# Kernel tuning notes

Hardware: AMD Instinct MI355X
Metric: run time of the kernel (lower is better)

## Reference

```python
import jax, jax.numpy as jnp
import numpy as np

N_SITE, D, PHYS, W = 40, 128, 2, 8  # sites, MPS bond dim, physical dim, MPO bond dim


def setup_inputs() -> dict:
    key = jax.random.key(0)
    k1, k2 = jax.random.split(key)
    # scale so 40-step transfer-matrix products stay O(1) in float32
    M = jax.random.normal(k1, (N_SITE, D, PHYS, D), jnp.float32) * (D * PHYS) ** -0.5
    H = jax.random.normal(k2, (N_SITE, W, W, PHYS, PHYS), jnp.float32) * (W * PHYS * PHYS) ** -0.5
    return {"M": M, "H": H}


def _energy(M, H):
    # <M|H|M> via left-to-right environment sweep. L has shape (D_bra, w, D_ket).
    L0 = jnp.zeros((D, W, D), M.dtype).at[0, 0, 0].set(1.0)  # open left boundary

    def step(L, mh):
        m, h = mh  # m: (a,i,p) bond,phys,bond ; h: (w,x,i,j) mpo-bond,mpo-bond,phys-out,phys-in
        T = jnp.einsum('awb,aip->wbip', L, m)      # absorb bra tensor (real, so no conj)
        T = jnp.einsum('wbip,wxij->bpxj', T, h)    # absorb MPO tensor
        L = jnp.einsum('bpxj,bjq->pxq', T, m)      # absorb ket tensor
        return L, None

    L, _ = jax.lax.scan(step, L0, (M, H))
    return L[0, W - 1, 0]  # open right boundary (MPO right boundary = last index)


def _norm(M):
    # <M|M> via transfer-matrix sweep. N has shape (D_bra, D_ket); stays PSD.
    N0 = jnp.zeros((D, D), M.dtype).at[0, 0].set(1.0)

    def step(N, m):
        T = jnp.einsum('ab,aip->bip', N, m)
        N = jnp.einsum('bip,biq->pq', T, m)
        return N, None

    N, _ = jax.lax.scan(step, N0, M)
    return N[0, 0]


def reference(M, H):
    EPS = 0.0
    NORM_LIM = 10000.0
    energy = _energy(M, H)
    norm = _norm(M)
    loss = energy / (norm + EPS)  # torch.real is identity for real dtype
    reg = jax.nn.relu(norm - NORM_LIM)
    return (energy, norm, loss, reg)
```

## Files before the change

### kernel.cpp

```cpp
#include <hip/hip_runtime.h>


#define D 128
#define W 8
#define NS 40
#define NPAIR 20
#define HALF2 10
#define MSZ (D * 2 * D)
#define HSZ (W * W * 2 * 2)
#define M2SZ (D * 4 * D)
#define H2SZ (W * W * 4 * 4)
#define LSZ (D * W * D)
#define NSZ (D * D)
#define T2SZ (D * W * D * 4)
#define TNSZ (4 * D * D)

#define OFF_M2 0
#define OFF_MR2 (OFF_M2 + NPAIR * M2SZ)
#define OFF_H2 (OFF_MR2 + HALF2 * M2SZ)
#define OFF_HR2 (OFF_H2 + NPAIR * H2SZ)
#define OFF_LL (OFF_HR2 + HALF2 * H2SZ)
#define OFF_LR (OFF_LL + LSZ)
#define OFF_NL (OFF_LR + LSZ)
#define OFF_NR (OFF_NL + NSZ)
#define OFF_T2L (OFF_NR + NSZ)
#define OFF_T2R (OFF_T2L + T2SZ)
#define OFF_TNL (OFF_T2R + T2SZ)
#define OFF_TNR (OFF_TNL + TNSZ)
#define OFF_PART (OFF_TNR + TNSZ)
#define OFF_PARTN (OFF_PART + 128)

__global__ __launch_bounds__(256) void k_prep1(const float* __restrict__ Min,
                                               const float* __restrict__ Hin,
                                               float* __restrict__ ws) {
    __shared__ float As[32 * 34];
    __shared__ float Bs[32 * 68];
    int bid = blockIdx.x, t = threadIdx.x;
    if (bid < 640) {
        int m = bid >> 5, tile = bid & 31;
        int r0 = (tile & 7) * 32, c0 = (tile >> 3) * 64;
        const float* A = Min + (2 * m) * MSZ;
        const float* B = Min + (2 * m + 1) * MSZ;
        float* C = ws + OFF_M2 + m * M2SZ;
        int ty = t >> 4, tx = t & 15;
        float a00 = 0, a01 = 0, a02 = 0, a03 = 0;
        float a10 = 0, a11 = 0, a12 = 0, a13 = 0;
        for (int c = 0; c < 4; ++c) {
            int k0 = c * 32;
            __syncthreads();
            {
                int rr = t >> 3, kq = t & 7;
                int row = r0 + rr;
                const float4 v = *(const float4*)&A[(row >> 1) * 256 + (row & 1) * 128 + k0 + kq * 4];
                float* dst = &As[kq * 136 + rr];
                dst[0] = v.x; dst[34] = v.y; dst[68] = v.z; dst[102] = v.w;
            }
#pragma unroll
            for (int u = 0; u < 2; ++u) {
                int e = u * 256 + t;
                int kk = e >> 4, cq = e & 15;
                const float4 v = *(const float4*)&B[(k0 + kk) * 256 + c0 + cq * 4];
                *(float4*)&Bs[kk * 68 + cq * 4] = v;
            }
            __syncthreads();
#pragma unroll 8
            for (int kk = 0; kk < 32; ++kk) {
                float2 av = *(float2*)&As[kk * 34 + 2 * ty];
                float4 bv = *(float4*)&Bs[kk * 68 + 4 * tx];
                a00 += av.x * bv.x; a01 += av.x * bv.y; a02 += av.x * bv.z; a03 += av.x * bv.w;
                a10 += av.y * bv.x; a11 += av.y * bv.y; a12 += av.y * bv.z; a13 += av.y * bv.w;
            }
        }
        int r = r0 + 2 * ty, cc = c0 + 4 * tx;
        int a = r >> 1, i2 = cc >> 7, cd = cc & 127;
        float4 v0; v0.x = a00; v0.y = a01; v0.z = a02; v0.w = a03;
        float4 v1; v1.x = a10; v1.y = a11; v1.z = a12; v1.w = a13;
        *(float4*)&C[a * 512 + (0 * 2 + i2) * 128 + cd] = v0;
        *(float4*)&C[a * 512 + (1 * 2 + i2) * 128 + cd] = v1;
    } else {
        for (int idx = t; idx < NPAIR * H2SZ; idx += 256) {
            int m = idx >> 10, r = idx & 1023;
            int w = r >> 7, x = (r >> 4) & 7, I = (r >> 2) & 3, J = r & 3;
            int i1 = I >> 1, i2 = I & 1, j1 = J >> 1, j2 = J & 1;
            const float* Ha = Hin + (2 * m) * HSZ;
            const float* Hb = Hin + (2 * m + 1) * HSZ;
            float s = 0.f;
#pragma unroll
            for (int v = 0; v < 8; ++v)
                s += Ha[w * 32 + v * 4 + i1 * 2 + j1] * Hb[v * 32 + x * 4 + i2 * 2 + j2];
            ws[OFF_H2 + idx] = s;
        }
    }
}

#define PR_MR (HALF2 * M2SZ)
#define PR_HR (PR_MR + HALF2 * H2SZ)
#define PR_TOT (PR_HR + 2 * LSZ + 2 * NSZ)
__global__ __launch_bounds__(256) void k_prep2(float* __restrict__ ws) {
    for (int idx = blockIdx.x * 256 + threadIdx.x; idx < PR_TOT; idx += gridDim.x * 256) {
        if (idx < PR_MR) {
            int kr = idx >> 16, r = idx & 65535;
            int a = r >> 9, I = (r >> 7) & 3, p = r & 127;
            ws[OFF_MR2 + idx] = ws[OFF_M2 + (19 - kr) * M2SZ + p * 512 + I * 128 + a];
        } else if (idx < PR_HR) {
            int e = idx - PR_MR;
            int kr = e >> 10, r = e & 1023;
            int w = r >> 7, x = (r >> 4) & 7, lo = r & 15;
            ws[OFF_HR2 + e] = ws[OFF_H2 + (19 - kr) * H2SZ + x * 128 + w * 16 + lo];
        } else {
            int e = idx - PR_HR;
            int off; float v = 0.f;
            if (e < LSZ)            { off = OFF_LL + e; if (e == 0) v = 1.f; }
            else if (e < 2 * LSZ)   { int r = e - LSZ; off = OFF_LR + r; if (r == (W - 1) * D) v = 1.f; }
            else if (e < 2 * LSZ + NSZ) { int r = e - 2 * LSZ; off = OFF_NL + r; if (r == 0) v = 1.f; }
            else                    { int r = e - 2 * LSZ - NSZ; off = OFF_NR + r; if (r == 0) v = 1.f; }
            ws[off] = v;
        }
    }
}

__global__ __launch_bounds__(512) void k_A2(float* __restrict__ ws, int k) {
    __shared__ __align__(16) float sm[9472];
    int bid = blockIdx.x, t = threadIdx.x;
    int z = t >> 8, tl = t & 255;
    if (bid < 128) {
        int side = bid >> 6;
        int eb = bid & 63;
        int b0 = (eb & 7) * 16;
        int p0 = (eb >> 3) * 16;
        const float* Lsrc = ws + (side ? OFF_LR : OFF_LL);
        const float* m2 = ws + (side ? OFF_MR2 : OFF_M2) + k * M2SZ;
        const float* h2 = ws + (side ? OFF_HR2 : OFF_H2) + k * H2SZ;
        float* T2 = ws + (side ? OFF_T2R : OFF_T2L);
        float* Ls = sm;
        float* ms = sm + 6400;
        float* hs = sm + 8448;
#pragma unroll
        for (int u = 0; u < 2; ++u) {
            int e = u * 512 + t;
            int w = e >> 7, I = (e >> 5) & 3, x = (e >> 2) & 7, J = e & 3;
            hs[e] = h2[w * 128 + x * 16 + I * 4 + J];
        }
        int b_l = tl & 15, p_l = tl >> 4;
        float acc[8][2];
#pragma unroll
        for (int w = 0; w < 8; ++w) { acc[w][0] = 0.f; acc[w][1] = 0.f; }
        int e0 = t, e1 = 512 + t;
        int la0 = e0 >> 5, lw0 = (e0 >> 2) & 7, lb0 = e0 & 3;
        int la1 = e1 >> 5, lw1 = (e1 >> 2) & 7, lb1 = e1 & 3;
        int maa = t >> 4, mI = (t >> 2) & 3, mpq = t & 3;
        float4 pl0 = *(const float4*)&Lsrc[la0 * 1024 + lw0 * 128 + b0 + lb0 * 4];
        float4 pl1 = *(const float4*)&Lsrc[la1 * 1024 + lw1 * 128 + b0 + lb1 * 4];
        float4 pm = *(const float4*)&m2[maa * 512 + mI * 128 + p0 + mpq * 4];
        for (int c = 0; c < 4; ++c) {
            __syncthreads();
            {
                float* d0 = &Ls[la0 * 200 + lb0 * 48 + lw0];
                d0[0] = pl0.x; d0[12] = pl0.y; d0[24] = pl0.z; d0[36] = pl0.w;
                float* d1 = &Ls[la1 * 200 + lb1 * 48 + lw1];
                d1[0] = pl1.x; d1[12] = pl1.y; d1[24] = pl1.z; d1[36] = pl1.w;
                *(float4*)&ms[maa * 64 + mI * 16 + mpq * 4] = pm;
            }
            if (c < 3) {
                int a0 = (c + 1) * 32;
                pl0 = *(const float4*)&Lsrc[(a0 + la0) * 1024 + lw0 * 128 + b0 + lb0 * 4];
                pl1 = *(const float4*)&Lsrc[(a0 + la1) * 1024 + lw1 * 128 + b0 + lb1 * 4];
                pm = *(const float4*)&m2[(a0 + maa) * 512 + mI * 128 + p0 + mpq * 4];
            }
            __syncthreads();
#pragma unroll 4
            for (int aa = 0; aa < 32; ++aa) {
                float4 l0 = *(float4*)&Ls[aa * 200 + b_l * 12];
                float4 l1 = *(float4*)&Ls[aa * 200 + b_l * 12 + 4];
                float lw[8] = {l0.x, l0.y, l0.z, l0.w, l1.x, l1.y, l1.z, l1.w};
                float mv0 = ms[aa * 64 + (2 * z) * 16 + p_l];
                float mv1 = ms[aa * 64 + (2 * z + 1) * 16 + p_l];
#pragma unroll
                for (int w = 0; w < 8; ++w) {
                    acc[w][0] += lw[w] * mv0;
                    acc[w][1] += lw[w] * mv1;
                }
            }
        }
        float o[32];
#pragma unroll
        for (int xJ = 0; xJ < 32; ++xJ) o[xJ] = 0.f;
#pragma unroll
        for (int w = 0; w < 8; ++w)
#pragma unroll
            for (int ii = 0; ii < 2; ++ii) {
                float tv = acc[w][ii];
                int wI = w * 4 + 2 * z + ii;
#pragma unroll
                for (int xJ = 0; xJ < 32; ++xJ) o[xJ] += tv * hs[wI * 32 + xJ];
            }
        __syncthreads();
        if (z == 1) {
#pragma unroll
            for (int j = 0; j < 8; ++j) {
                float4 v; v.x = o[j * 4]; v.y = o[j * 4 + 1];
                v.z = o[j * 4 + 2]; v.w = o[j * 4 + 3];
                *(float4*)&sm[tl * 32 + j * 4] = v;
            }
        }
        __syncthreads();
        if (z == 0) {
#pragma unroll
            for (int j = 0; j < 32; ++j) o[j] += sm[tl * 32 + j];
            int b = b0 + b_l, p = p0 + p_l;
#pragma unroll
            for (int x = 0; x < 8; ++x) {
                float4 v; v.x = o[x * 4]; v.y = o[x * 4 + 1];
                v.z = o[x * 4 + 2]; v.w = o[x * 4 + 3];
                *(float4*)&T2[p * 4096 + x * 512 + b * 4] = v;
            }
        }
    } else {
        int g = (bid - 128) * 2 + z;
        int side = g >> 5;
        int nn = g & 31;
        int b0 = (nn & 3) * 32;
        int c0 = (nn >> 2) * 64;
        const float* Nsrc = ws + (side ? OFF_NR : OFF_NL);
        const float* m2 = ws + (side ? OFF_MR2 : OFF_M2) + k * M2SZ;
        float* Tn = ws + (side ? OFF_TNR : OFF_TNL);
        float* As = sm + z * 3264;
        float* Bs = sm + z * 3264 + 1056;
        int ty = tl >> 4, tx = tl & 15;
        float a00 = 0, a01 = 0, a02 = 0, a03 = 0;
        float a10 = 0, a11 = 0, a12 = 0, a13 = 0;
        for (int c = 0; c < 4; ++c) {
            int a0 = c * 32;
            __syncthreads();
#pragma unroll
            for (int u = 0; u < 4; ++u) {
                int e = u * 256 + tl;
                int kk = e >> 5, col = e & 31;
                As[kk * 33 + col] = Nsrc[(a0 + kk) * 128 + b0 + col];
            }
#pragma unroll
            for (int u = 0; u < 8; ++u) {
                int e = u * 256 + tl;
                int kk = e >> 6, col = e & 63;
                Bs[kk * 68 + col] = m2[(a0 + kk) * 512 + c0 + col];
            }
            __syncthreads();
#pragma unroll 8
            for (int kk = 0; kk < 32; ++kk) {
                float av0 = As[kk * 33 + 2 * ty], av1 = As[kk * 33 + 2 * ty + 1];
                float4 bv = *(float4*)&Bs[kk * 68 + 4 * tx];
                a00 += av0 * bv.x; a01 += av0 * bv.y; a02 += av0 * bv.z; a03 += av0 * bv.w;
                a10 += av1 * bv.x; a11 += av1 * bv.y; a12 += av1 * bv.z; a13 += av1 * bv.w;
            }
        }
        int b_ = b0 + 2 * ty;
        float rowv[2][4] = {{a00, a01, a02, a03}, {a10, a11, a12, a13}};
#pragma unroll
        for (int jj = 0; jj < 4; ++jj) {
            int col = c0 + 4 * tx + jj;
            int I = col >> 7, p = col & 127;
            Tn[I * 16384 + p * 128 + b_] = rowv[0][jj];
            Tn[I * 16384 + p * 128 + b_ + 1] = rowv[1][jj];
        }
    }
}

__global__ __launch_bounds__(512) void k_B2(float* __restrict__ ws, int k) {
    __shared__ __align__(16) float sm[8576];
    int bid = blockIdx.x, t = threadIdx.x;
    int z = t >> 8, tl = t & 255;
    int ty = tl >> 4, tx = tl & 15;
    float a00 = 0, a01 = 0, a02 = 0, a03 = 0;
    float a10 = 0, a11 = 0, a12 = 0, a13 = 0;
    float* As = sm + z * 3264;
    float* Bs = sm + z * 3264 + 1088;
    float* red = sm + 6528;
    if (bid < 128) {
        int side = bid >> 6;
        int eb = bid & 63;
        int r0 = (eb & 31) * 32;
        int c0 = (eb >> 5) * 64;
        const float* A = ws + (side ? OFF_T2R : OFF_T2L);
        const float* B = ws + (side ? OFF_MR2 : OFF_M2) + k * M2SZ;
        float* C = ws + (side ? OFF_LR : OFF_LL);
        int rr = tl >> 3, kq = tl & 7;
        int kkb0 = tl >> 4, cq0 = tl & 15;
        int kkb1 = (256 + tl) >> 4, cq1 = tl & 15;
        int k0 = (z * 8) * 32;
        float4 pa = *(const float4*)&A[(r0 + rr) * 512 + k0 + kq * 4];
        int row0 = k0 + kkb0, row1 = k0 + kkb1;
        float4 pb0 = *(const float4*)&B[(row0 >> 2) * 512 + (row0 & 3) * 128 + c0 + cq0 * 4];
        float4 pb1 = *(const float4*)&B[(row1 >> 2) * 512 + (row1 & 3) * 128 + c0 + cq1 * 4];
        for (int c = 0; c < 8; ++c) {
            __syncthreads();
            {
                float* dst = &As[kq * 136 + rr];
                dst[0] = pa.x; dst[34] = pa.y; dst[68] = pa.z; dst[102] = pa.w;
                *(float4*)&Bs[kkb0 * 68 + cq0 * 4] = pb0;
                *(float4*)&Bs[kkb1 * 68 + cq1 * 4] = pb1;
            }
            if (c < 7) {
                int kn = (z * 8 + c + 1) * 32;
                pa = *(const float4*)&A[(r0 + rr) * 512 + kn + kq * 4];
                int r0n = kn + kkb0, r1n = kn + kkb1;
                pb0 = *(const float4*)&B[(r0n >> 2) * 512 + (r0n & 3) * 128 + c0 + cq0 * 4];
                pb1 = *(const float4*)&B[(r1n >> 2) * 512 + (r1n & 3) * 128 + c0 + cq1 * 4];
            }
            __syncthreads();
#pragma unroll 8
            for (int kk = 0; kk < 32; ++kk) {
                float av0 = As[kk * 34 + 2 * ty], av1 = As[kk * 34 + 2 * ty + 1];
                float4 bv = *(float4*)&Bs[kk * 68 + 4 * tx];
                a00 += av0 * bv.x; a01 += av0 * bv.y; a02 += av0 * bv.z; a03 += av0 * bv.w;
                a10 += av1 * bv.x; a11 += av1 * bv.y; a12 += av1 * bv.z; a13 += av1 * bv.w;
            }
        }
        __syncthreads();
        if (z == 1) {
            float4 v0; v0.x = a00; v0.y = a01; v0.z = a02; v0.w = a03;
            float4 v1; v1.x = a10; v1.y = a11; v1.z = a12; v1.w = a13;
            *(float4*)&red[tl * 8] = v0;
            *(float4*)&red[tl * 8 + 4] = v1;
        }
        __syncthreads();
        if (z == 0) {
            float4 v0 = *(float4*)&red[tl * 8];
            float4 v1 = *(float4*)&red[tl * 8 + 4];
            a00 += v0.x; a01 += v0.y; a02 += v0.z; a03 += v0.w;
            a10 += v1.x; a11 += v1.y; a12 += v1.z; a13 += v1.w;
            int r = r0 + 2 * ty, cc = c0 + 4 * tx;
            float4 w0; w0.x = a00; w0.y = a01; w0.z = a02; w0.w = a03;
            float4 w1; w1.x = a10; w1.y = a11; w1.z = a12; w1.w = a13;
            *(float4*)&C[(r >> 3) * 1024 + (r & 7) * 128 + cc] = w0;
            *(float4*)&C[((r + 1) >> 3) * 1024 + ((r + 1) & 7) * 128 + cc] = w1;
        }
    } else if (bid < 144) {
        int g = bid - 128;
        int side = g >> 3;
        int nn = g & 7;
        int r0 = (nn & 3) * 32;
        int c0 = (nn >> 2) * 64;
        const float* A = ws + (side ? OFF_TNR : OFF_TNL);
        const float* B = ws + (side ? OFF_MR2 : OFF_M2) + k * M2SZ;
        float* C = ws + (side ? OFF_NR : OFF_NL);
        for (int c = 0; c < 8; ++c) {
            int cg = z * 8 + c;
            int Ic = cg >> 2, bc = (cg & 3) * 32;
            __syncthreads();
            {
                int rr = tl >> 3, kq = tl & 7;
                const float4 v = *(const float4*)&A[Ic * 16384 + (r0 + rr) * 128 + bc + kq * 4];
                float* dst = &As[kq * 136 + rr];
                dst[0] = v.x; dst[34] = v.y; dst[68] = v.z; dst[102] = v.w;
            }
#pragma unroll
            for (int u = 0; u < 2; ++u) {
                int e = u * 256 + tl;
                int kk = e >> 4, cq = e & 15;
                const float4 v = *(const float4*)&B[(bc + kk) * 512 + Ic * 128 + c0 + cq * 4];
                *(float4*)&Bs[kk * 68 + cq * 4] = v;
            }
            __syncthreads();
#pragma unroll 8
            for (int kk = 0; kk < 32; ++kk) {
                float av0 = As[kk * 34 + 2 * ty], av1 = As[kk * 34 + 2 * ty + 1];
                float4 bv = *(float4*)&Bs[kk * 68 + 4 * tx];
                a00 += av0 * bv.x; a01 += av0 * bv.y; a02 += av0 * bv.z; a03 += av0 * bv.w;
                a10 += av1 * bv.x; a11 += av1 * bv.y; a12 += av1 * bv.z; a13 += av1 * bv.w;
            }
        }
        __syncthreads();
        if (z == 1) {
            float4 v0; v0.x = a00; v0.y = a01; v0.z = a02; v0.w = a03;
            float4 v1; v1.x = a10; v1.y = a11; v1.z = a12; v1.w = a13;
            *(float4*)&red[tl * 8] = v0;
            *(float4*)&red[tl * 8 + 4] = v1;
        }
        __syncthreads();
        if (z == 0) {
            float4 v0 = *(float4*)&red[tl * 8];
            float4 v1 = *(float4*)&red[tl * 8 + 4];
            a00 += v0.x; a01 += v0.y; a02 += v0.z; a03 += v0.w;
            a10 += v1.x; a11 += v1.y; a12 += v1.z; a13 += v1.w;
            int r = r0 + 2 * ty, cc = c0 + 4 * tx;
            float4 w0; w0.x = a00; w0.y = a01; w0.z = a02; w0.w = a03;
            float4 w1; w1.x = a10; w1.y = a11; w1.z = a12; w1.w = a13;
            *(float4*)&C[r * 128 + cc] = w0;
            *(float4*)&C[(r + 1) * 128 + cc] = w1;
        }
    }
}

__global__ __launch_bounds__(256) void k_dot(float* __restrict__ ws) {
    __shared__ float se[256], sn[256];
    int bid = blockIdx.x, t = threadIdx.x;
    const float* LL = ws + OFF_LL;
    const float* LR = ws + OFF_LR;
    float e = 0.f;
#pragma unroll
    for (int u = 0; u < 4; ++u) {
        int i = bid * 1024 + u * 256 + t;
        e += LL[i] * LR[i];
    }
    float n = 0.f;
    if (t < 128) {
        int i = bid * 128 + t;
        n = ws[OFF_NL + i] * ws[OFF_NR + i];
    }
    se[t] = e;
    sn[t] = n;
    __syncthreads();
    for (int s = 128; s > 0; s >>= 1) {
        if (t < s) { se[t] += se[t + s]; sn[t] += sn[t + s]; }
        __syncthreads();
    }
    if (t == 0) {
        ws[OFF_PART + bid] = se[0];
        ws[OFF_PARTN + bid] = sn[0];
    }
}

__global__ __launch_bounds__(256) void k_loss(const float* __restrict__ ws,
                                              float* __restrict__ out) {
    __shared__ float se[128], sn[128];
    int t = threadIdx.x;
    if (t < 128) {
        se[t] = ws[OFF_PART + t];
        sn[t] = ws[OFF_PARTN + t];
    }
    __syncthreads();
    for (int s = 64; s > 0; s >>= 1) {
        if (t < s) { se[t] += se[t + s]; sn[t] += sn[t + s]; }
        __syncthreads();
    }
    if (t == 0) {
        float E = se[0], Nm = sn[0];
        out[0] = E;
        out[1] = Nm;
        out[2] = E / Nm;
        out[3] = fmaxf(Nm - 10000.0f, 0.0f);
    }
}

extern "C" void kernel_launch(void* const* d_in, const int* in_sizes, int n_in,
                              void* d_out, int out_size, void* d_ws, size_t ws_size,
                              hipStream_t stream) {
    const float* Min = (const float*)d_in[0];
    const float* Hin = (const float*)d_in[1];
    float* ws = (float*)d_ws;
    float* out = (float*)d_out;
    (void)in_sizes; (void)n_in; (void)out_size; (void)ws_size;

    k_prep1<<<dim3(641), dim3(256), 0, stream>>>(Min, Hin, ws);
    k_prep2<<<dim3(640), dim3(256), 0, stream>>>(ws);
    for (int k = 0; k < HALF2; ++k) {
        k_A2<<<dim3(160), dim3(512), 0, stream>>>(ws, k);
        k_B2<<<dim3(144), dim3(512), 0, stream>>>(ws, k);
    }
    k_dot<<<dim3(128), dim3(256), 0, stream>>>(ws);
    k_loss<<<dim3(1), dim3(256), 0, stream>>>(ws, out);
}
```

Baseline: 385.9 us.

## Split contraction dimension across warp groups in k_A2 and k_B2 with larger register tiles

In k_A2 the two 256-thread halves now each take half of the bond-index reduction and compute all four physical indices, instead of splitting by physical index. Their partial sums are reduced through shared memory before a single MPO contraction, so the h-tensor contraction runs once per output rather than twice. In k_B2 the energy-path GEMM uses eight 64-thread groups, each with a 4x8 register tile over its own K slice, followed by an eight-way shared-memory reduction. This raises the FMA-to-load ratio and cuts redundant work, at the cost of much more shared memory and a larger reduction step, which may lower occupancy.

```diff
diff --git a/kernel.cpp b/kernel.cpp
--- a/kernel.cpp
+++ b/kernel.cpp
@@ -120,7 +120,7 @@
 }
 
 __global__ __launch_bounds__(512) void k_A2(float* __restrict__ ws, int k) {
-    __shared__ __align__(16) float sm[9472];
+    __shared__ __align__(16) float sm[17920];
     int bid = blockIdx.x, t = threadIdx.x;
     int z = t >> 8, tl = t & 255;
     if (bid < 128) {
@@ -132,9 +132,9 @@
         const float* m2 = ws + (side ? OFF_MR2 : OFF_M2) + k * M2SZ;
         const float* h2 = ws + (side ? OFF_HR2 : OFF_H2) + k * H2SZ;
         float* T2 = ws + (side ? OFF_T2R : OFF_T2L);
-        float* Ls = sm;
-        float* ms = sm + 6400;
-        float* hs = sm + 8448;
+        float* Ls = sm + z * 6400;
+        float* ms = sm + 12800 + z * 2048;
+        float* hs = sm + 16896;
 #pragma unroll
         for (int u = 0; u < 2; ++u) {
             int e = u * 512 + t;
@@ -142,71 +142,95 @@
             hs[e] = h2[w * 128 + x * 16 + I * 4 + J];
         }
         int b_l = tl & 15, p_l = tl >> 4;
-        float acc[8][2];
-#pragma unroll
-        for (int w = 0; w < 8; ++w) { acc[w][0] = 0.f; acc[w][1] = 0.f; }
-        int e0 = t, e1 = 512 + t;
-        int la0 = e0 >> 5, lw0 = (e0 >> 2) & 7, lb0 = e0 & 3;
-        int la1 = e1 >> 5, lw1 = (e1 >> 2) & 7, lb1 = e1 & 3;
-        int maa = t >> 4, mI = (t >> 2) & 3, mpq = t & 3;
-        float4 pl0 = *(const float4*)&Lsrc[la0 * 1024 + lw0 * 128 + b0 + lb0 * 4];
-        float4 pl1 = *(const float4*)&Lsrc[la1 * 1024 + lw1 * 128 + b0 + lb1 * 4];
-        float4 pm = *(const float4*)&m2[maa * 512 + mI * 128 + p0 + mpq * 4];
-        for (int c = 0; c < 4; ++c) {
-            __syncthreads();
-            {
-                float* d0 = &Ls[la0 * 200 + lb0 * 48 + lw0];
-                d0[0] = pl0.x; d0[12] = pl0.y; d0[24] = pl0.z; d0[36] = pl0.w;
-                float* d1 = &Ls[la1 * 200 + lb1 * 48 + lw1];
-                d1[0] = pl1.x; d1[12] = pl1.y; d1[24] = pl1.z; d1[36] = pl1.w;
-                *(float4*)&ms[maa * 64 + mI * 16 + mpq * 4] = pm;
-            }
-            if (c < 3) {
-                int a0 = (c + 1) * 32;
-                pl0 = *(const float4*)&Lsrc[(a0 + la0) * 1024 + lw0 * 128 + b0 + lb0 * 4];
-                pl1 = *(const float4*)&Lsrc[(a0 + la1) * 1024 + lw1 * 128 + b0 + lb1 * 4];
-                pm = *(const float4*)&m2[(a0 + maa) * 512 + mI * 128 + p0 + mpq * 4];
+        float acc[8][4];
+#pragma unroll
+        for (int w = 0; w < 8; ++w)
+#pragma unroll
+            for (int I = 0; I < 4; ++I) acc[w][I] = 0.f;
+        int la[4], lw[4], lb[4], maa[2], mI[2], mpq[2];
+#pragma unroll
+        for (int u = 0; u < 4; ++u) {
+            int e = u * 256 + tl;
+            la[u] = e >> 5; lw[u] = (e >> 2) & 7; lb[u] = e & 3;
+        }
+#pragma unroll
+        for (int u = 0; u < 2; ++u) {
+            int e = u * 256 + tl;
+            maa[u] = e >> 4; mI[u] = (e >> 2) & 3; mpq[u] = e & 3;
+        }
+        float4 pl[4], pm[2];
+        {
+            int a0 = z * 64;
+#pragma unroll
+            for (int u = 0; u < 4; ++u)
+                pl[u] = *(const float4*)&Lsrc[(a0 + la[u]) * 1024 + lw[u] * 128 + b0 + lb[u] * 4];
+#pragma unroll
+            for (int u = 0; u < 2; ++u)
+                pm[u] = *(const float4*)&m2[(a0 + maa[u]) * 512 + mI[u] * 128 + p0 + mpq[u] * 4];
+        }
+        for (int c = 0; c < 2; ++c) {
+            __syncthreads();
+#pragma unroll
+            for (int u = 0; u < 4; ++u) {
+                float* dst = &Ls[la[u] * 200 + lb[u] * 48 + lw[u]];
+                dst[0] = pl[u].x; dst[12] = pl[u].y; dst[24] = pl[u].z; dst[36] = pl[u].w;
+            }
+#pragma unroll
+            for (int u = 0; u < 2; ++u) {
+                int base = maa[u] * 64 + mpq[u] * 16 + mI[u];
+                ms[base] = pm[u].x; ms[base + 4] = pm[u].y;
+                ms[base + 8] = pm[u].z; ms[base + 12] = pm[u].w;
+            }
+            if (c == 0) {
+                int a0 = z * 64 + 32;
+#pragma unroll
+                for (int u = 0; u < 4; ++u)
+                    pl[u] = *(const float4*)&Lsrc[(a0 + la[u]) * 1024 + lw[u] * 128 + b0 + lb[u] * 4];
+#pragma unroll
+                for (int u = 0; u < 2; ++u)
+                    pm[u] = *(const float4*)&m2[(a0 + maa[u]) * 512 + mI[u] * 128 + p0 + mpq[u] * 4];
             }
             __syncthreads();
 #pragma unroll 4
             for (int aa = 0; aa < 32; ++aa) {
                 float4 l0 = *(float4*)&Ls[aa * 200 + b_l * 12];
                 float4 l1 = *(float4*)&Ls[aa * 200 + b_l * 12 + 4];
-                float lw[8] = {l0.x, l0.y, l0.z, l0.w, l1.x, l1.y, l1.z, l1.w};
-                float mv0 = ms[aa * 64 + (2 * z) * 16 + p_l];
-                float mv1 = ms[aa * 64 + (2 * z + 1) * 16 + p_l];
+                float4 mv = *(float4*)&ms[aa * 64 + p_l * 4];
+                float lv[8] = {l0.x, l0.y, l0.z, l0.w, l1.x, l1.y, l1.z, l1.w};
 #pragma unroll
                 for (int w = 0; w < 8; ++w) {
-                    acc[w][0] += lw[w] * mv0;
-                    acc[w][1] += lw[w] * mv1;
+                    acc[w][0] += lv[w] * mv.x;
+                    acc[w][1] += lv[w] * mv.y;
+                    acc[w][2] += lv[w] * mv.z;
+                    acc[w][3] += lv[w] * mv.w;
                 }
             }
         }
-        float o[32];
-#pragma unroll
-        for (int xJ = 0; xJ < 32; ++xJ) o[xJ] = 0.f;
-#pragma unroll
-        for (int w = 0; w < 8; ++w)
-#pragma unroll
-            for (int ii = 0; ii < 2; ++ii) {
-                float tv = acc[w][ii];
-                int wI = w * 4 + 2 * z + ii;
+        __syncthreads();
+        float* red = sm;
+        if (z == 1) {
+#pragma unroll
+            for (int w = 0; w < 8; ++w) {
+                float4 v; v.x = acc[w][0]; v.y = acc[w][1]; v.z = acc[w][2]; v.w = acc[w][3];
+                *(float4*)&red[tl * 32 + w * 4] = v;
+            }
+        }
+        __syncthreads();
+        if (z == 0) {
+#pragma unroll
+            for (int w = 0; w < 8; ++w) {
+                float4 v = *(float4*)&red[tl * 32 + w * 4];
+                acc[w][0] += v.x; acc[w][1] += v.y; acc[w][2] += v.z; acc[w][3] += v.w;
+            }
+            float o[32];
+#pragma unroll
+            for (int xJ = 0; xJ < 32; ++xJ) o[xJ] = 0.f;
+#pragma unroll
+            for (int wI = 0; wI < 32; ++wI) {
+                float tv = acc[wI >> 2][wI & 3];
 #pragma unroll
                 for (int xJ = 0; xJ < 32; ++xJ) o[xJ] += tv * hs[wI * 32 + xJ];
             }
-        __syncthreads();
-        if (z == 1) {
-#pragma unroll
-            for (int j = 0; j < 8; ++j) {
-                float4 v; v.x = o[j * 4]; v.y = o[j * 4 + 1];
-                v.z = o[j * 4 + 2]; v.w = o[j * 4 + 3];
-                *(float4*)&sm[tl * 32 + j * 4] = v;
-            }
-        }
-        __syncthreads();
-        if (z == 0) {
-#pragma unroll
-            for (int j = 0; j < 32; ++j) o[j] += sm[tl * 32 + j];
             int b = b0 + b_l, p = p0 + p_l;
 #pragma unroll
             for (int x = 0; x < 8; ++x) {
@@ -266,15 +290,8 @@
 }
 
 __global__ __launch_bounds__(512) void k_B2(float* __restrict__ ws, int k) {
-    __shared__ __align__(16) float sm[8576];
+    __shared__ __align__(16) float sm[26624];
     int bid = blockIdx.x, t = threadIdx.x;
-    int z = t >> 8, tl = t & 255;
-    int ty = tl >> 4, tx = tl & 15;
-    float a00 = 0, a01 = 0, a02 = 0, a03 = 0;
-    float a10 = 0, a11 = 0, a12 = 0, a13 = 0;
-    float* As = sm + z * 3264;
-    float* Bs = sm + z * 3264 + 1088;
-    float* red = sm + 6528;
     if (bid < 128) {
         int side = bid >> 6;
         int eb = bid & 63;
@@ -283,58 +300,112 @@
         const float* A = ws + (side ? OFF_T2R : OFF_T2L);
         const float* B = ws + (side ? OFF_MR2 : OFF_M2) + k * M2SZ;
         float* C = ws + (side ? OFF_LR : OFF_LL);
-        int rr = tl >> 3, kq = tl & 7;
-        int kkb0 = tl >> 4, cq0 = tl & 15;
-        int kkb1 = (256 + tl) >> 4, cq1 = tl & 15;
-        int k0 = (z * 8) * 32;
-        float4 pa = *(const float4*)&A[(r0 + rr) * 512 + k0 + kq * 4];
-        int row0 = k0 + kkb0, row1 = k0 + kkb1;
-        float4 pb0 = *(const float4*)&B[(row0 >> 2) * 512 + (row0 & 3) * 128 + c0 + cq0 * 4];
-        float4 pb1 = *(const float4*)&B[(row1 >> 2) * 512 + (row1 & 3) * 128 + c0 + cq1 * 4];
-        for (int c = 0; c < 8; ++c) {
-            __syncthreads();
-            {
-                float* dst = &As[kq * 136 + rr];
-                dst[0] = pa.x; dst[34] = pa.y; dst[68] = pa.z; dst[102] = pa.w;
-                *(float4*)&Bs[kkb0 * 68 + cq0 * 4] = pb0;
-                *(float4*)&Bs[kkb1 * 68 + cq1 * 4] = pb1;
-            }
-            if (c < 7) {
-                int kn = (z * 8 + c + 1) * 32;
-                pa = *(const float4*)&A[(r0 + rr) * 512 + kn + kq * 4];
-                int r0n = kn + kkb0, r1n = kn + kkb1;
-                pb0 = *(const float4*)&B[(r0n >> 2) * 512 + (r0n & 3) * 128 + c0 + cq0 * 4];
-                pb1 = *(const float4*)&B[(r1n >> 2) * 512 + (r1n & 3) * 128 + c0 + cq1 * 4];
+        int z = t >> 6, tl = t & 63;
+        int ty = tl >> 3, tx = tl & 7;
+        float acc[4][8];
+#pragma unroll
+        for (int j = 0; j < 4; ++j)
+#pragma unroll
+            for (int q = 0; q < 8; ++q) acc[j][q] = 0.f;
+        float* As = sm + z * 3328;
+        float* Bs = sm + z * 3328 + 1152;
+        int arr[4], akq[4], bkk[8], bcq[8];
+#pragma unroll
+        for (int u = 0; u < 4; ++u) {
+            int e = u * 64 + tl;
+            arr[u] = e >> 3; akq[u] = e & 7;
+        }
+#pragma unroll
+        for (int u = 0; u < 8; ++u) {
+            int e = u * 64 + tl;
+            bkk[u] = e >> 4; bcq[u] = e & 15;
+        }
+        float4 pa[4], pb[8];
+        {
+            int k0 = z * 64;
+#pragma unroll
+            for (int u = 0; u < 4; ++u)
+                pa[u] = *(const float4*)&A[(r0 + arr[u]) * 512 + k0 + akq[u] * 4];
+#pragma unroll
+            for (int u = 0; u < 8; ++u) {
+                int row = k0 + bkk[u];
+                pb[u] = *(const float4*)&B[(row >> 2) * 512 + (row & 3) * 128 + c0 + bcq[u] * 4];
+            }
+        }
+        for (int c = 0; c < 2; ++c) {
+            __syncthreads();
+#pragma unroll
+            for (int u = 0; u < 4; ++u) {
+                float* dst = &As[(akq[u] * 4) * 36 + arr[u]];
+                dst[0] = pa[u].x; dst[36] = pa[u].y; dst[72] = pa[u].z; dst[108] = pa[u].w;
+            }
+#pragma unroll
+            for (int u = 0; u < 8; ++u)
+                *(float4*)&Bs[bkk[u] * 68 + bcq[u] * 4] = pb[u];
+            if (c == 0) {
+                int k0 = z * 64 + 32;
+#pragma unroll
+                for (int u = 0; u < 4; ++u)
+                    pa[u] = *(const float4*)&A[(r0 + arr[u]) * 512 + k0 + akq[u] * 4];
+#pragma unroll
+                for (int u = 0; u < 8; ++u) {
+                    int row = k0 + bkk[u];
+                    pb[u] = *(const float4*)&B[(row >> 2) * 512 + (row & 3) * 128 + c0 + bcq[u] * 4];
+                }
             }
             __syncthreads();
 #pragma unroll 8
             for (int kk = 0; kk < 32; ++kk) {
-                float av0 = As[kk * 34 + 2 * ty], av1 = As[kk * 34 + 2 * ty + 1];
-                float4 bv = *(float4*)&Bs[kk * 68 + 4 * tx];
-                a00 += av0 * bv.x; a01 += av0 * bv.y; a02 += av0 * bv.z; a03 += av0 * bv.w;
-                a10 += av1 * bv.x; a11 += av1 * bv.y; a12 += av1 * bv.z; a13 += av1 * bv.w;
-            }
-        }
-        __syncthreads();
-        if (z == 1) {
-            float4 v0; v0.x = a00; v0.y = a01; v0.z = a02; v0.w = a03;
-            float4 v1; v1.x = a10; v1.y = a11; v1.z = a12; v1.w = a13;
-            *(float4*)&red[tl * 8] = v0;
-            *(float4*)&red[tl * 8 + 4] = v1;
-        }
-        __syncthreads();
-        if (z == 0) {
-            float4 v0 = *(float4*)&red[tl * 8];
-            float4 v1 = *(float4*)&red[tl * 8 + 4];
-            a00 += v0.x; a01 += v0.y; a02 += v0.z; a03 += v0.w;
-            a10 += v1.x; a11 += v1.y; a12 += v1.z; a13 += v1.w;
-            int r = r0 + 2 * ty, cc = c0 + 4 * tx;
-            float4 w0; w0.x = a00; w0.y = a01; w0.z = a02; w0.w = a03;
-            float4 w1; w1.x = a10; w1.y = a11; w1.z = a12; w1.w = a13;
-            *(float4*)&C[(r >> 3) * 1024 + (r & 7) * 128 + cc] = w0;
-            *(float4*)&C[((r + 1) >> 3) * 1024 + ((r + 1) & 7) * 128 + cc] = w1;
+                float4 av = *(float4*)&As[kk * 36 + ty * 4];
+                float4 bv0 = *(float4*)&Bs[kk * 68 + tx * 8];
+                float4 bv1 = *(float4*)&Bs[kk * 68 + tx * 8 + 4];
+                float avv[4] = {av.x, av.y, av.z, av.w};
+#pragma unroll
+                for (int j = 0; j < 4; ++j) {
+                    acc[j][0] += avv[j] * bv0.x; acc[j][1] += avv[j] * bv0.y;
+                    acc[j][2] += avv[j] * bv0.z; acc[j][3] += avv[j] * bv0.w;
+                    acc[j][4] += avv[j] * bv1.x; acc[j][5] += avv[j] * bv1.y;
+                    acc[j][6] += avv[j] * bv1.z; acc[j][7] += avv[j] * bv1.w;
+                }
+            }
+        }
+        __syncthreads();
+        float* red = sm;
+#pragma unroll
+        for (int j = 0; j < 4; ++j) {
+#pragma unroll
+            for (int qq = 0; qq < 2; ++qq) {
+                float4 v;
+                v.x = acc[j][qq * 4]; v.y = acc[j][qq * 4 + 1];
+                v.z = acc[j][qq * 4 + 2]; v.w = acc[j][qq * 4 + 3];
+                *(float4*)&red[z * 2048 + tl * 32 + j * 8 + qq * 4] = v;
+            }
+        }
+        __syncthreads();
+        {
+            int pos = t >> 3;
+            int vi0 = (t & 7) * 4;
+            float4 s;
+            s.x = 0.f; s.y = 0.f; s.z = 0.f; s.w = 0.f;
+#pragma unroll
+            for (int zz = 0; zz < 8; ++zz) {
+                float4 v = *(float4*)&red[zz * 2048 + pos * 32 + vi0];
+                s.x += v.x; s.y += v.y; s.z += v.z; s.w += v.w;
+            }
+            int j = vi0 >> 3;
+            int q0 = vi0 & 7;
+            int r = r0 + (pos >> 3) * 4 + j;
+            int cc = c0 + (pos & 7) * 8 + q0;
+            *(float4*)&C[(r >> 3) * 1024 + (r & 7) * 128 + cc] = s;
         }
     } else if (bid < 144) {
+        int z = t >> 8, tl = t & 255;
+        int ty = tl >> 4, tx = tl & 15;
+        float a00 = 0, a01 = 0, a02 = 0, a03 = 0;
+        float a10 = 0, a11 = 0, a12 = 0, a13 = 0;
+        float* As = sm + z * 3264;
+        float* Bs = sm + z * 3264 + 1088;
+        float* red = sm + 6528;
         int g = bid - 128;
         int side = g >> 3;
         int nn = g & 7;
```

After: 429.3 us. +11.2%, slower.

## Split reduction dimension across blocks with partial-sum buffers to double grid size

Applied to the files above, without the earlier changes.

The energy sweep kernels now split their contraction (reduction) dimension in half across twice as many blocks. Each half writes a separate partial buffer for T2 and L, and the consumer adds the two partials when it loads them. The intent is to fill more of the MI355X's compute units, since the previous grids of 160/144 blocks left many CUs idle in these latency-bound per-step launches. In exchange, each step reads twice as many global loads for L/T2 and the workspace grows.

```diff
diff --git a/kernel.cpp b/kernel.cpp
--- a/kernel.cpp
+++ b/kernel.cpp
@@ -19,15 +19,17 @@
 #define OFF_MR2 (OFF_M2 + NPAIR * M2SZ)
 #define OFF_H2 (OFF_MR2 + HALF2 * M2SZ)
 #define OFF_HR2 (OFF_H2 + NPAIR * H2SZ)
-#define OFF_LL (OFF_HR2 + HALF2 * H2SZ)
-#define OFF_LR (OFF_LL + LSZ)
-#define OFF_NL (OFF_LR + LSZ)
-#define OFF_NR (OFF_NL + NSZ)
-#define OFF_T2L (OFF_NR + NSZ)
-#define OFF_T2R (OFF_T2L + T2SZ)
-#define OFF_TNL (OFF_T2R + T2SZ)
-#define OFF_TNR (OFF_TNL + TNSZ)
-#define OFF_PART (OFF_TNR + TNSZ)
+#define OFF_L (OFF_HR2 + HALF2 * H2SZ)
+#define LP(side, kh) (OFF_L + ((side) * 2 + (kh)) * LSZ)
+#define OFF_N (OFF_L + 4 * LSZ)
+#define OFF_NL OFF_N
+#define OFF_NR (OFF_N + NSZ)
+#define OFF_T2 (OFF_N + 2 * NSZ)
+#define T2P(side, ah) (OFF_T2 + ((side) * 2 + (ah)) * T2SZ)
+#define OFF_TN (OFF_T2 + 4 * T2SZ)
+#define OFF_TNL OFF_TN
+#define OFF_TNR (OFF_TN + TNSZ)
+#define OFF_PART (OFF_TN + 2 * TNSZ)
 #define OFF_PARTN (OFF_PART + 128)
 
 __global__ __launch_bounds__(256) void k_prep1(const float* __restrict__ Min,
@@ -95,7 +97,7 @@
 
 #define PR_MR (HALF2 * M2SZ)
 #define PR_HR (PR_MR + HALF2 * H2SZ)
-#define PR_TOT (PR_HR + 2 * LSZ + 2 * NSZ)
+#define PR_TOT (PR_HR + 4 * LSZ + 2 * NSZ)
 __global__ __launch_bounds__(256) void k_prep2(float* __restrict__ ws) {
     for (int idx = blockIdx.x * 256 + threadIdx.x; idx < PR_TOT; idx += gridDim.x * 256) {
         if (idx < PR_MR) {
@@ -110,10 +112,12 @@
         } else {
             int e = idx - PR_HR;
             int off; float v = 0.f;
-            if (e < LSZ)            { off = OFF_LL + e; if (e == 0) v = 1.f; }
-            else if (e < 2 * LSZ)   { int r = e - LSZ; off = OFF_LR + r; if (r == (W - 1) * D) v = 1.f; }
-            else if (e < 2 * LSZ + NSZ) { int r = e - 2 * LSZ; off = OFF_NL + r; if (r == 0) v = 1.f; }
-            else                    { int r = e - 2 * LSZ - NSZ; off = OFF_NR + r; if (r == 0) v = 1.f; }
+            if (e < LSZ)            { off = LP(0, 0) + e; if (e == 0) v = 1.f; }
+            else if (e < 2 * LSZ)   { off = LP(0, 1) + (e - LSZ); }
+            else if (e < 3 * LSZ)   { int r = e - 2 * LSZ; off = LP(1, 0) + r; if (r == (W - 1) * D) v = 1.f; }
+            else if (e < 4 * LSZ)   { off = LP(1, 1) + (e - 3 * LSZ); }
+            else if (e < 4 * LSZ + NSZ) { int r = e - 4 * LSZ; off = OFF_NL + r; if (r == 0) v = 1.f; }
+            else                    { int r = e - 4 * LSZ - NSZ; off = OFF_NR + r; if (r == 0) v = 1.f; }
             ws[off] = v;
         }
     }
@@ -123,15 +127,18 @@
     __shared__ __align__(16) float sm[9472];
     int bid = blockIdx.x, t = threadIdx.x;
     int z = t >> 8, tl = t & 255;
-    if (bid < 128) {
-        int side = bid >> 6;
-        int eb = bid & 63;
+    if (bid < 256) {
+        int side = bid >> 7;
+        int e2 = bid & 127;
+        int ah = e2 >> 6;
+        int eb = e2 & 63;
         int b0 = (eb & 7) * 16;
         int p0 = (eb >> 3) * 16;
-        const float* Lsrc = ws + (side ? OFF_LR : OFF_LL);
+        const float* La = ws + LP(side, 0);
+        const float* Lb = ws + LP(side, 1);
         const float* m2 = ws + (side ? OFF_MR2 : OFF_M2) + k * M2SZ;
         const float* h2 = ws + (side ? OFF_HR2 : OFF_H2) + k * H2SZ;
-        float* T2 = ws + (side ? OFF_T2R : OFF_T2L);
+        float* T2 = ws + T2P(side, ah);
         float* Ls = sm;
         float* ms = sm + 6400;
         float* hs = sm + 8448;
@@ -149,22 +156,33 @@
         int la0 = e0 >> 5, lw0 = (e0 >> 2) & 7, lb0 = e0 & 3;
         int la1 = e1 >> 5, lw1 = (e1 >> 2) & 7, lb1 = e1 & 3;
         int maa = t >> 4, mI = (t >> 2) & 3, mpq = t & 3;
-        float4 pl0 = *(const float4*)&Lsrc[la0 * 1024 + lw0 * 128 + b0 + lb0 * 4];
-        float4 pl1 = *(const float4*)&Lsrc[la1 * 1024 + lw1 * 128 + b0 + lb1 * 4];
-        float4 pm = *(const float4*)&m2[maa * 512 + mI * 128 + p0 + mpq * 4];
-        for (int c = 0; c < 4; ++c) {
+        int abase = ah * 64;
+        float4 pa0, pa1, pb0, pb1, pm;
+        {
+            int a0 = abase;
+            pa0 = *(const float4*)&La[(a0 + la0) * 1024 + lw0 * 128 + b0 + lb0 * 4];
+            pb0 = *(const float4*)&Lb[(a0 + la0) * 1024 + lw0 * 128 + b0 + lb0 * 4];
+            pa1 = *(const float4*)&La[(a0 + la1) * 1024 + lw1 * 128 + b0 + lb1 * 4];
+            pb1 = *(const float4*)&Lb[(a0 + la1) * 1024 + lw1 * 128 + b0 + lb1 * 4];
+            pm = *(const float4*)&m2[(a0 + maa) * 512 + mI * 128 + p0 + mpq * 4];
+        }
+        for (int c = 0; c < 2; ++c) {
             __syncthreads();
             {
                 float* d0 = &Ls[la0 * 200 + lb0 * 48 + lw0];
-                d0[0] = pl0.x; d0[12] = pl0.y; d0[24] = pl0.z; d0[36] = pl0.w;
+                d0[0] = pa0.x + pb0.x; d0[12] = pa0.y + pb0.y;
+                d0[24] = pa0.z + pb0.z; d0[36] = pa0.w + pb0.w;
                 float* d1 = &Ls[la1 * 200 + lb1 * 48 + lw1];
-                d1[0] = pl1.x; d1[12] = pl1.y; d1[24] = pl1.z; d1[36] = pl1.w;
+                d1[0] = pa1.x + pb1.x; d1[12] = pa1.y + pb1.y;
+                d1[24] = pa1.z + pb1.z; d1[36] = pa1.w + pb1.w;
                 *(float4*)&ms[maa * 64 + mI * 16 + mpq * 4] = pm;
             }
-            if (c < 3) {
-                int a0 = (c + 1) * 32;
-                pl0 = *(const float4*)&Lsrc[(a0 + la0) * 1024 + lw0 * 128 + b0 + lb0 * 4];
-                pl1 = *(const float4*)&Lsrc[(a0 + la1) * 1024 + lw1 * 128 + b0 + lb1 * 4];
+            if (c == 0) {
+                int a0 = abase + 32;
+                pa0 = *(const float4*)&La[(a0 + la0) * 1024 + lw0 * 128 + b0 + lb0 * 4];
+                pb0 = *(const float4*)&Lb[(a0 + la0) * 1024 + lw0 * 128 + b0 + lb0 * 4];
+                pa1 = *(const float4*)&La[(a0 + la1) * 1024 + lw1 * 128 + b0 + lb1 * 4];
+                pb1 = *(const float4*)&Lb[(a0 + la1) * 1024 + lw1 * 128 + b0 + lb1 * 4];
                 pm = *(const float4*)&m2[(a0 + maa) * 512 + mI * 128 + p0 + mpq * 4];
             }
             __syncthreads();
@@ -216,7 +234,7 @@
             }
         }
     } else {
-        int g = (bid - 128) * 2 + z;
+        int g = (bid - 256) * 2 + z;
         int side = g >> 5;
         int nn = g & 31;
         int b0 = (nn & 3) * 32;
@@ -275,33 +293,40 @@
     float* As = sm + z * 3264;
     float* Bs = sm + z * 3264 + 1088;
     float* red = sm + 6528;
-    if (bid < 128) {
-        int side = bid >> 6;
-        int eb = bid & 63;
+    if (bid < 256) {
+        int side = bid >> 7;
+        int e2 = bid & 127;
+        int kh = e2 >> 6;
+        int eb = e2 & 63;
         int r0 = (eb & 31) * 32;
         int c0 = (eb >> 5) * 64;
-        const float* A = ws + (side ? OFF_T2R : OFF_T2L);
+        const float* Aa = ws + T2P(side, 0);
+        const float* Ab = ws + T2P(side, 1);
         const float* B = ws + (side ? OFF_MR2 : OFF_M2) + k * M2SZ;
-        float* C = ws + (side ? OFF_LR : OFF_LL);
+        float* C = ws + LP(side, kh);
         int rr = tl >> 3, kq = tl & 7;
         int kkb0 = tl >> 4, cq0 = tl & 15;
         int kkb1 = (256 + tl) >> 4, cq1 = tl & 15;
-        int k0 = (z * 8) * 32;
-        float4 pa = *(const float4*)&A[(r0 + rr) * 512 + k0 + kq * 4];
+        int cbase = kh * 8 + z * 4;
+        int k0 = cbase * 32;
+        float4 paa = *(const float4*)&Aa[(r0 + rr) * 512 + k0 + kq * 4];
+        float4 pab = *(const float4*)&Ab[(r0 + rr) * 512 + k0 + kq * 4];
         int row0 = k0 + kkb0, row1 = k0 + kkb1;
         float4 pb0 = *(const float4*)&B[(row0 >> 2) * 512 + (row0 & 3) * 128 + c0 + cq0 * 4];
         float4 pb1 = *(const float4*)&B[(row1 >> 2) * 512 + (row1 & 3) * 128 + c0 + cq1 * 4];
-        for (int c = 0; c < 8; ++c) {
+        for (int c = 0; c < 4; ++c) {
             __syncthreads();
             {
                 float* dst = &As[kq * 136 + rr];
-                dst[0] = pa.x; dst[34] = pa.y; dst[68] = pa.z; dst[102] = pa.w;
+                dst[0] = paa.x + pab.x; dst[34] = paa.y + pab.y;
+                dst[68] = paa.z + pab.z; dst[102] = paa.w + pab.w;
                 *(float4*)&Bs[kkb0 * 68 + cq0 * 4] = pb0;
                 *(float4*)&Bs[kkb1 * 68 + cq1 * 4] = pb1;
             }
-            if (c < 7) {
-                int kn = (z * 8 + c + 1) * 32;
-                pa = *(const float4*)&A[(r0 + rr) * 512 + kn + kq * 4];
+            if (c < 3) {
+                int kn = (cbase + c + 1) * 32;
+                paa = *(const float4*)&Aa[(r0 + rr) * 512 + kn + kq * 4];
+                pab = *(const float4*)&Ab[(r0 + rr) * 512 + kn + kq * 4];
                 int r0n = kn + kkb0, r1n = kn + kkb1;
                 pb0 = *(const float4*)&B[(r0n >> 2) * 512 + (r0n & 3) * 128 + c0 + cq0 * 4];
                 pb1 = *(const float4*)&B[(r1n >> 2) * 512 + (r1n & 3) * 128 + c0 + cq1 * 4];
@@ -334,8 +359,8 @@
             *(float4*)&C[(r >> 3) * 1024 + (r & 7) * 128 + cc] = w0;
             *(float4*)&C[((r + 1) >> 3) * 1024 + ((r + 1) & 7) * 128 + cc] = w1;
         }
-    } else if (bid < 144) {
-        int g = bid - 128;
+    } else if (bid < 272) {
+        int g = bid - 256;
         int side = g >> 3;
         int nn = g & 7;
         int r0 = (nn & 3) * 32;
@@ -394,13 +419,15 @@
 __global__ __launch_bounds__(256) void k_dot(float* __restrict__ ws) {
     __shared__ float se[256], sn[256];
     int bid = blockIdx.x, t = threadIdx.x;
-    const float* LL = ws + OFF_LL;
-    const float* LR = ws + OFF_LR;
+    const float* LLa = ws + LP(0, 0);
+    const float* LLb = ws + LP(0, 1);
+    const float* LRa = ws + LP(1, 0);
+    const float* LRb = ws + LP(1, 1);
     float e = 0.f;
 #pragma unroll
     for (int u = 0; u < 4; ++u) {
         int i = bid * 1024 + u * 256 + t;
-        e += LL[i] * LR[i];
+        e += (LLa[i] + LLb[i]) * (LRa[i] + LRb[i]);
     }
     float n = 0.f;
     if (t < 128) {
@@ -454,8 +481,8 @@
     k_prep1<<<dim3(641), dim3(256), 0, stream>>>(Min, Hin, ws);
     k_prep2<<<dim3(640), dim3(256), 0, stream>>>(ws);
     for (int k = 0; k < HALF2; ++k) {
-        k_A2<<<dim3(160), dim3(512), 0, stream>>>(ws, k);
-        k_B2<<<dim3(144), dim3(512), 0, stream>>>(ws, k);
+        k_A2<<<dim3(288), dim3(512), 0, stream>>>(ws, k);
+        k_B2<<<dim3(272), dim3(512), 0, stream>>>(ws, k);
     }
     k_dot<<<dim3(128), dim3(256), 0, stream>>>(ws);
     k_loss<<<dim3(1), dim3(256), 0, stream>>>(ws, out);
```

Measured after the change: 459.1 us. 1.19x slower.

## Split the contraction's a-dimension across thread halves and defer the MPO contraction

Applied to the files above, without the earlier changes.

The first-stage block in k_A2 is restructured so each half of the 512-thread block reduces over a different half of the bond index a, with its own shared-memory L and M tiles. Each thread now accumulates all four physical I values and reads one float4 of M per step. The two halves are summed through shared memory before the H contraction, which now runs only in the z==0 half. This halves the number of serial chunk iterations and removes the per-half duplicated L reads. In exchange it roughly doubles shared-memory use, raises register pressure, and leaves half the threads idle during the H stage.

```diff
diff --git a/kernel.cpp b/kernel.cpp
--- a/kernel.cpp
+++ b/kernel.cpp
@@ -120,7 +120,7 @@
 }
 
 __global__ __launch_bounds__(512) void k_A2(float* __restrict__ ws, int k) {
-    __shared__ __align__(16) float sm[9472];
+    __shared__ __align__(16) float sm[17920];
     int bid = blockIdx.x, t = threadIdx.x;
     int z = t >> 8, tl = t & 255;
     if (bid < 128) {
@@ -132,9 +132,9 @@
         const float* m2 = ws + (side ? OFF_MR2 : OFF_M2) + k * M2SZ;
         const float* h2 = ws + (side ? OFF_HR2 : OFF_H2) + k * H2SZ;
         float* T2 = ws + (side ? OFF_T2R : OFF_T2L);
-        float* Ls = sm;
-        float* ms = sm + 6400;
-        float* hs = sm + 8448;
+        float* Ls = sm + z * 6400;
+        float* ms = sm + 12800 + z * 2048;
+        float* hs = sm + 16896;
 #pragma unroll
         for (int u = 0; u < 2; ++u) {
             int e = u * 512 + t;
@@ -142,71 +142,95 @@
             hs[e] = h2[w * 128 + x * 16 + I * 4 + J];
         }
         int b_l = tl & 15, p_l = tl >> 4;
-        float acc[8][2];
-#pragma unroll
-        for (int w = 0; w < 8; ++w) { acc[w][0] = 0.f; acc[w][1] = 0.f; }
-        int e0 = t, e1 = 512 + t;
-        int la0 = e0 >> 5, lw0 = (e0 >> 2) & 7, lb0 = e0 & 3;
-        int la1 = e1 >> 5, lw1 = (e1 >> 2) & 7, lb1 = e1 & 3;
-        int maa = t >> 4, mI = (t >> 2) & 3, mpq = t & 3;
-        float4 pl0 = *(const float4*)&Lsrc[la0 * 1024 + lw0 * 128 + b0 + lb0 * 4];
-        float4 pl1 = *(const float4*)&Lsrc[la1 * 1024 + lw1 * 128 + b0 + lb1 * 4];
-        float4 pm = *(const float4*)&m2[maa * 512 + mI * 128 + p0 + mpq * 4];
-        for (int c = 0; c < 4; ++c) {
-            __syncthreads();
-            {
-                float* d0 = &Ls[la0 * 200 + lb0 * 48 + lw0];
-                d0[0] = pl0.x; d0[12] = pl0.y; d0[24] = pl0.z; d0[36] = pl0.w;
-                float* d1 = &Ls[la1 * 200 + lb1 * 48 + lw1];
-                d1[0] = pl1.x; d1[12] = pl1.y; d1[24] = pl1.z; d1[36] = pl1.w;
-                *(float4*)&ms[maa * 64 + mI * 16 + mpq * 4] = pm;
-            }
-            if (c < 3) {
-                int a0 = (c + 1) * 32;
-                pl0 = *(const float4*)&Lsrc[(a0 + la0) * 1024 + lw0 * 128 + b0 + lb0 * 4];
-                pl1 = *(const float4*)&Lsrc[(a0 + la1) * 1024 + lw1 * 128 + b0 + lb1 * 4];
-                pm = *(const float4*)&m2[(a0 + maa) * 512 + mI * 128 + p0 + mpq * 4];
+        float acc[8][4];
+#pragma unroll
+        for (int w = 0; w < 8; ++w)
+#pragma unroll
+            for (int I = 0; I < 4; ++I) acc[w][I] = 0.f;
+        int la[4], lw[4], lb[4], maa[2], mI[2], mpq[2];
+#pragma unroll
+        for (int u = 0; u < 4; ++u) {
+            int e = u * 256 + tl;
+            la[u] = e >> 5; lw[u] = (e >> 2) & 7; lb[u] = e & 3;
+        }
+#pragma unroll
+        for (int u = 0; u < 2; ++u) {
+            int e = u * 256 + tl;
+            maa[u] = e >> 4; mI[u] = (e >> 2) & 3; mpq[u] = e & 3;
+        }
+        float4 pl[4], pm[2];
+        {
+            int a0 = z * 64;
+#pragma unroll
+            for (int u = 0; u < 4; ++u)
+                pl[u] = *(const float4*)&Lsrc[(a0 + la[u]) * 1024 + lw[u] * 128 + b0 + lb[u] * 4];
+#pragma unroll
+            for (int u = 0; u < 2; ++u)
+                pm[u] = *(const float4*)&m2[(a0 + maa[u]) * 512 + mI[u] * 128 + p0 + mpq[u] * 4];
+        }
+        for (int c = 0; c < 2; ++c) {
+            __syncthreads();
+#pragma unroll
+            for (int u = 0; u < 4; ++u) {
+                float* dst = &Ls[la[u] * 200 + lb[u] * 48 + lw[u]];
+                dst[0] = pl[u].x; dst[12] = pl[u].y; dst[24] = pl[u].z; dst[36] = pl[u].w;
+            }
+#pragma unroll
+            for (int u = 0; u < 2; ++u) {
+                int base = maa[u] * 64 + mpq[u] * 16 + mI[u];
+                ms[base] = pm[u].x; ms[base + 4] = pm[u].y;
+                ms[base + 8] = pm[u].z; ms[base + 12] = pm[u].w;
+            }
+            if (c == 0) {
+                int a0 = z * 64 + 32;
+#pragma unroll
+                for (int u = 0; u < 4; ++u)
+                    pl[u] = *(const float4*)&Lsrc[(a0 + la[u]) * 1024 + lw[u] * 128 + b0 + lb[u] * 4];
+#pragma unroll
+                for (int u = 0; u < 2; ++u)
+                    pm[u] = *(const float4*)&m2[(a0 + maa[u]) * 512 + mI[u] * 128 + p0 + mpq[u] * 4];
             }
             __syncthreads();
 #pragma unroll 4
             for (int aa = 0; aa < 32; ++aa) {
                 float4 l0 = *(float4*)&Ls[aa * 200 + b_l * 12];
                 float4 l1 = *(float4*)&Ls[aa * 200 + b_l * 12 + 4];
-                float lw[8] = {l0.x, l0.y, l0.z, l0.w, l1.x, l1.y, l1.z, l1.w};
-                float mv0 = ms[aa * 64 + (2 * z) * 16 + p_l];
-                float mv1 = ms[aa * 64 + (2 * z + 1) * 16 + p_l];
+                float4 mv = *(float4*)&ms[aa * 64 + p_l * 4];
+                float lv[8] = {l0.x, l0.y, l0.z, l0.w, l1.x, l1.y, l1.z, l1.w};
 #pragma unroll
                 for (int w = 0; w < 8; ++w) {
-                    acc[w][0] += lw[w] * mv0;
-                    acc[w][1] += lw[w] * mv1;
+                    acc[w][0] += lv[w] * mv.x;
+                    acc[w][1] += lv[w] * mv.y;
+                    acc[w][2] += lv[w] * mv.z;
+                    acc[w][3] += lv[w] * mv.w;
                 }
             }
         }
-        float o[32];
-#pragma unroll
-        for (int xJ = 0; xJ < 32; ++xJ) o[xJ] = 0.f;
-#pragma unroll
-        for (int w = 0; w < 8; ++w)
-#pragma unroll
-            for (int ii = 0; ii < 2; ++ii) {
-                float tv = acc[w][ii];
-                int wI = w * 4 + 2 * z + ii;
+        __syncthreads();
+        float* red = sm;
+        if (z == 1) {
+#pragma unroll
+            for (int w = 0; w < 8; ++w) {
+                float4 v; v.x = acc[w][0]; v.y = acc[w][1]; v.z = acc[w][2]; v.w = acc[w][3];
+                *(float4*)&red[tl * 32 + w * 4] = v;
+            }
+        }
+        __syncthreads();
+        if (z == 0) {
+#pragma unroll
+            for (int w = 0; w < 8; ++w) {
+                float4 v = *(float4*)&red[tl * 32 + w * 4];
+                acc[w][0] += v.x; acc[w][1] += v.y; acc[w][2] += v.z; acc[w][3] += v.w;
+            }
+            float o[32];
+#pragma unroll
+            for (int xJ = 0; xJ < 32; ++xJ) o[xJ] = 0.f;
+#pragma unroll
+            for (int wI = 0; wI < 32; ++wI) {
+                float tv = acc[wI >> 2][wI & 3];
 #pragma unroll
                 for (int xJ = 0; xJ < 32; ++xJ) o[xJ] += tv * hs[wI * 32 + xJ];
             }
-        __syncthreads();
-        if (z == 1) {
-#pragma unroll
-            for (int j = 0; j < 8; ++j) {
-                float4 v; v.x = o[j * 4]; v.y = o[j * 4 + 1];
-                v.z = o[j * 4 + 2]; v.w = o[j * 4 + 3];
-                *(float4*)&sm[tl * 32 + j * 4] = v;
-            }
-        }
-        __syncthreads();
-        if (z == 0) {
-#pragma unroll
-            for (int j = 0; j < 32; ++j) o[j] += sm[tl * 32 + j];
             int b = b0 + b_l, p = p0 + p_l;
 #pragma unroll
             for (int x = 0; x < 8; ++x) {
```

Result: no change. 387.6 us (+0.4%).
